# Performance work log

Hardware: AMD Instinct MI355X
Metric: run time of the kernel (lower is better)

## Reference

```python
import jax, jax.numpy as jnp
import numpy as np

TEMPERATURE = 0.08
NEG = -9e15  # matches torch masked_fill value
EPS = 1e-8   # F.cosine_similarity eps


def setup_inputs() -> dict:
    key = jax.random.key(0)
    inputs = jax.random.normal(key, (8192, 512), dtype=jnp.float32)
    return {"inputs": inputs}


def reference(inputs):
    N = inputs.shape[0]
    # cosine similarity via normalize + GEMM (avoids NxNxD broadcast)
    norms = jnp.maximum(jnp.linalg.norm(inputs, axis=-1, keepdims=True), EPS)
    z = inputs / norms
    sim = z @ z.T  # [N, N]
    # mask self-similarity BEFORE temperature scaling (as in the torch code)
    diag = jnp.eye(N, dtype=bool)
    sim = jnp.where(diag, NEG, sim)
    sim = sim / TEMPERATURE
    # positive of row i is column (i - N//2) % N (eye rolled by N//2 along dim 0)
    idx = jnp.arange(N)
    pos_idx = (idx - N // 2) % N
    pos = jnp.take_along_axis(sim, pos_idx[:, None], axis=1)[:, 0]  # [N]
    nll = jnp.mean(-pos + jax.scipy.special.logsumexp(sim, axis=-1))
    # rank of the positive: counting-based equivalent of
    # cat([pos, sim_masked]).argsort(desc).argmin() with stable ties
    masked = sim.at[idx, pos_idx].set(NEG)
    positive_ranking = jnp.sum(masked > pos[:, None], axis=-1)  # [N] int
    return positive_ranking, nll
```

## Files before the change

kernel.cpp:

```cpp
#include <hip/hip_runtime.h>
#include <cstdint>
#include <cstddef>

#define NROW 8192
#define DIM  512
#define HALF 4096
#define INV_T 12.5f
#define LDSW 64

typedef __bf16 bf16x8  __attribute__((ext_vector_type(8)));
typedef float  floatx4 __attribute__((ext_vector_type(4)));

__device__ __forceinline__ float bf2f_lo(unsigned u) { return __uint_as_float(u << 16); }
__device__ __forceinline__ float bf2f_hi(unsigned u) { return __uint_as_float(u & 0xffff0000u); }
__device__ __forceinline__ unsigned short f2bf(float f) {
    unsigned u = __float_as_uint(f);
    u += 0x7fffu + ((u >> 16) & 1u);
    return (unsigned short)(u >> 16);
}

__device__ __forceinline__ void atom_addf(float* p, float v) {
    __hip_atomic_fetch_add(p, v, __ATOMIC_RELAXED, __HIP_MEMORY_SCOPE_AGENT);
}

__global__ void knormpos(const float* __restrict__ x, unsigned short* __restrict__ z,
                         float* __restrict__ pos, float* __restrict__ sumexp,
                         float* __restrict__ cnt, float* __restrict__ nll_acc,
                         int* __restrict__ done) {
    int id = blockIdx.x * 256 + threadIdx.x;
    if (id < NROW) { sumexp[id] = 0.f; cnt[id] = 0.f; }
    if (id == 0) { nll_acc[0] = 0.f; done[0] = 0; }

    __shared__ __align__(16) unsigned short zs[4][512];

    const int w = threadIdx.x >> 6, lane = threadIdx.x & 63;
    const int row = blockIdx.x * 2 + (w & 1) + (w >> 1) * HALF;

    const float* xr = x + (size_t)row * DIM + lane * 8;
    float4 v0 = ((const float4*)xr)[0];
    float4 v1 = ((const float4*)xr)[1];
    float ss = v0.x*v0.x + v0.y*v0.y + v0.z*v0.z + v0.w*v0.w
             + v1.x*v1.x + v1.y*v1.y + v1.z*v1.z + v1.w*v1.w;
    #pragma unroll
    for (int m = 1; m < 64; m <<= 1) ss += __shfl_xor(ss, m);
    float inv = 1.0f / fmaxf(sqrtf(ss), 1e-8f);
    uint4 o;
    o.x = (unsigned)f2bf(v0.x * inv) | ((unsigned)f2bf(v0.y * inv) << 16);
    o.y = (unsigned)f2bf(v0.z * inv) | ((unsigned)f2bf(v0.w * inv) << 16);
    o.z = (unsigned)f2bf(v1.x * inv) | ((unsigned)f2bf(v1.y * inv) << 16);
    o.w = (unsigned)f2bf(v1.z * inv) | ((unsigned)f2bf(v1.w * inv) << 16);
    *(uint4*)(&zs[w][lane * 8]) = o;
    int sl = (lane & 56) | ((lane & 7) ^ (row & 7));
    *(uint4*)(z + (size_t)row * DIM + sl * 8) = o;
    __syncthreads();

    if (w < 2) {
        uint4 a = *(const uint4*)(&zs[w][lane * 8]);
        uint4 b = *(const uint4*)(&zs[w + 2][lane * 8]);
        float s = bf2f_lo(a.x)*bf2f_lo(b.x) + bf2f_hi(a.x)*bf2f_hi(b.x)
                + bf2f_lo(a.y)*bf2f_lo(b.y) + bf2f_hi(a.y)*bf2f_hi(b.y)
                + bf2f_lo(a.z)*bf2f_lo(b.z) + bf2f_hi(a.z)*bf2f_hi(b.z)
                + bf2f_lo(a.w)*bf2f_lo(b.w) + bf2f_hi(a.w)*bf2f_hi(b.w);
        #pragma unroll
        for (int m = 1; m < 64; m <<= 1) s += __shfl_xor(s, m);
        if (lane == 0) {
            const int r = blockIdx.x * 2 + w;
            pos[r] = s;
            pos[r + HALF] = s;
        }
    }
}

__global__ __launch_bounds__(256) void kgemm(const unsigned short* __restrict__ z,
                                             const float* __restrict__ pos,
                                             float* __restrict__ sumexp,
                                             float* __restrict__ cnt) {
    __shared__ __align__(16) unsigned short As[128 * LDSW];
    __shared__ __align__(16) unsigned short Bs[128 * LDSW];

    const int b = blockIdx.x;
    int I = 0;
    while (b >= 516 * (I + 1) - 32 * (I + 1) * (I + 1)) ++I;
    const int lb = b - (516 * I - 32 * I * I);
    int bi, bj;
    if (lb < 36) {
        int ti = 0;
        while (lb >= 8 * (ti + 1) - (ti + 1) * ti / 2) ++ti;
        const int tj = ti + (lb - (8 * ti - ti * (ti - 1) / 2));
        bi = I * 8 + ti;
        bj = I * 8 + tj;
    } else {
        const int o = lb - 36;
        const int J = I + 1 + (o >> 6);
        bi = I * 8 + ((o & 63) >> 3);
        bj = J * 8 + (o & 7);
    }
    const int r0 = bi * 128;
    const int c0 = bj * 128;
    const bool offdiag = (bi != bj);

    const int t = threadIdx.x;
    const int w = t >> 6, lane = t & 63;
    const int wm = w >> 1, wn = w & 1;

    floatx4 acc[4][4];
    #pragma unroll
    for (int i = 0; i < 4; ++i)
        #pragma unroll
        for (int j = 0; j < 4; ++j)
            acc[i][j] = floatx4{0.f, 0.f, 0.f, 0.f};

    const int lrow8 = lane >> 3;
    const int lcol  = (lane & 7) * 8;

    for (int kk = 0; kk < 8; ++kk) {
        const int k0 = kk * 64;
        #pragma unroll
        for (int it = 0; it < 4; ++it) {
            const int c = it * 4 + w;
            const unsigned short* gA = z + (size_t)(r0 + c * 8 + lrow8) * DIM + k0 + lcol;
            const unsigned short* gB = z + (size_t)(c0 + c * 8 + lrow8) * DIM + k0 + lcol;
            __builtin_amdgcn_global_load_lds(
                (const __attribute__((address_space(1))) unsigned int*)gA,
                (__attribute__((address_space(3))) unsigned int*)(As + c * 512),
                16, 0, 0);
            __builtin_amdgcn_global_load_lds(
                (const __attribute__((address_space(1))) unsigned int*)gB,
                (__attribute__((address_space(3))) unsigned int*)(Bs + c * 512),
                16, 0, 0);
        }
        __syncthreads();
        const int q = lane >> 4, cid16 = lane & 15;
        #pragma unroll
        for (int ks = 0; ks < 2; ++ks) {
            bf16x8 af[4], bfv[4];
            #pragma unroll
            for (int f = 0; f < 4; ++f) {
                const int ar = wm * 64 + f * 16 + cid16;
                const int br = wn * 64 + f * 16 + cid16;
                const int pa = (4 * ks + q) ^ (ar & 7);
                const int pb = (4 * ks + q) ^ (br & 7);
                af[f]  = *(const bf16x8*)(As + ar * LDSW + pa * 8);
                bfv[f] = *(const bf16x8*)(Bs + br * LDSW + pb * 8);
            }
            #pragma unroll
            for (int fm = 0; fm < 4; ++fm)
                #pragma unroll
                for (int fn = 0; fn < 4; ++fn)
                    acc[fm][fn] = __builtin_amdgcn_mfma_f32_16x16x32_bf16(
                        af[fm], bfv[fn], acc[fm][fn], 0, 0, 0);
        }
        __syncthreads();
    }

    const int rgrp = lane >> 4;
    const int cid  = lane & 15;

    #pragma unroll
    for (int fm = 0; fm < 4; ++fm) {
        #pragma unroll
        for (int r = 0; r < 4; ++r) {
            const int li = wm * 64 + fm * 16 + rgrp * 4 + r;
            const int i  = r0 + li;
            const float pv = pos[i];
            const int pj = (i + HALF) & (NROW - 1);
            float esum = 0.f, csum = 0.f;
            #pragma unroll
            for (int fn = 0; fn < 4; ++fn) {
                const int j = c0 + wn * 64 + fn * 16 + cid;
                const float s = acc[fm][fn][r];
                const bool diag = (j == i);
                esum += diag ? 0.f : __expf(s * INV_T - INV_T);
                csum += (!diag && (j != pj) && (s > pv)) ? 1.f : 0.f;
            }
            #pragma unroll
            for (int m = 1; m < 16; m <<= 1) {
                esum += __shfl_xor(esum, m);
                csum += __shfl_xor(csum, m);
            }
            if (cid == 0) {
                atom_addf(&sumexp[i], esum);
                atom_addf(&cnt[i], csum);
            }
        }
    }

    if (offdiag) {
        #pragma unroll
        for (int fn = 0; fn < 4; ++fn) {
            const int lj = wn * 64 + fn * 16 + cid;
            const int j  = c0 + lj;
            const float pvc = pos[j];
            const int pjc = (j + HALF) & (NROW - 1);
            float ec = 0.f, cc = 0.f;
            #pragma unroll
            for (int fm = 0; fm < 4; ++fm) {
                #pragma unroll
                for (int r = 0; r < 4; ++r) {
                    const int i = r0 + wm * 64 + fm * 16 + rgrp * 4 + r;
                    const float s = acc[fm][fn][r];
                    ec += __expf(s * INV_T - INV_T);
                    cc += ((i != pjc) && (s > pvc)) ? 1.f : 0.f;
                }
            }
            ec += __shfl_xor(ec, 16); ec += __shfl_xor(ec, 32);
            cc += __shfl_xor(cc, 16); cc += __shfl_xor(cc, 32);
            if (rgrp == 0) {
                atom_addf(&sumexp[j], ec);
                atom_addf(&cnt[j], cc);
            }
        }
    }
}

__global__ void NCELoss_3126736191777_kernel(const float* __restrict__ cnt,
                                             const float* __restrict__ sumexp,
                                             const float* __restrict__ pos,
                                             float* __restrict__ out,
                                             float* __restrict__ nll_acc,
                                             int* __restrict__ done) {
    __shared__ float red[4];
    const int t = threadIdx.x;
    const int r = blockIdx.x * 256 + t;
    float c = cnt[r], se = sumexp[r], p = pos[r];
    float v;
    if (p != p || fabsf(p) > 1.05f) v = 60000.0f;
    else if (se == 0.0f)            v = 40000.0f;
    else if (c < 0.0f)              v = 25000.0f;
    else                            v = c;
    out[r] = v;
    float local = -p * INV_T + INV_T + __logf(se);
    #pragma unroll
    for (int m = 1; m < 64; m <<= 1) local += __shfl_xor(local, m);
    if ((t & 63) == 0) red[t >> 6] = local;
    __syncthreads();
    if (t == 0) {
        atom_addf(nll_acc, red[0] + red[1] + red[2] + red[3]);
        __threadfence();
        int ticket = __hip_atomic_fetch_add(done, 1, __ATOMIC_ACQ_REL,
                                            __HIP_MEMORY_SCOPE_AGENT);
        if (ticket == (int)gridDim.x - 1) {
            __threadfence();
            out[NROW] = nll_acc[0] / (float)NROW;
        }
    }
}

extern "C" void kernel_launch(void* const* d_in, const int* in_sizes, int n_in,
                              void* d_out, int out_size, void* d_ws, size_t ws_size,
                              hipStream_t stream) {
    (void)in_sizes; (void)n_in; (void)out_size; (void)ws_size;
    const float* x = (const float*)d_in[0];

    char* base = (char*)d_ws;
    float* pos     = (float*)(base);
    float* sumexp  = (float*)(base + (size_t)NROW * 4);
    float* cnt     = (float*)(base + (size_t)NROW * 8);
    float* nll_acc = (float*)(base + (size_t)NROW * 12);
    int*   done    = (int*)(base + (size_t)NROW * 12 + 64);
    unsigned short* z = (unsigned short*)(base + (size_t)NROW * 12 + 4096);
    float* out = (float*)d_out;

    knormpos<<<NROW / 4, 256, 0, stream>>>(x, z, pos, sumexp, cnt, nll_acc, done);
    kgemm<<<2080, 256, 0, stream>>>(z, pos, sumexp, cnt);
    NCELoss_3126736191777_kernel<<<NROW / 256, 256, 0, stream>>>(cnt, sumexp, pos, out, nll_acc, done);
}
```

Baseline: 191.6 us.

## Load GEMM fragments directly from global memory and reduce row sums via LDS

The GEMM kernel drops its LDS staging and per-k-step barriers. Each lane now reads its bf16 MFMA fragments straight from global memory, and the swizzled z store is replaced by a plain row-major layout. The epilogue caches pos values in LDS and computes row and column exp/count partials in a single pass. Row partials are reduced through an LDS table so each row gets one atomic instead of one per 16-lane group. This removes barrier and LDS-copy overhead and cuts row atomics, but relies on L1/L2 for reuse, with 16-byte strided global loads that lose the shared-tile data reuse.

New measurement: 203.2 us. 6.0% more time.

```diff
diff --git a/kernel.cpp b/kernel.cpp
--- a/kernel.cpp
+++ b/kernel.cpp
@@ -6,7 +6,6 @@
 #define DIM  512
 #define HALF 4096
 #define INV_T 12.5f
-#define LDSW 64
 
 typedef __bf16 bf16x8  __attribute__((ext_vector_type(8)));
 typedef float  floatx4 __attribute__((ext_vector_type(4)));
@@ -50,8 +49,7 @@
     o.z = (unsigned)f2bf(v1.x * inv) | ((unsigned)f2bf(v1.y * inv) << 16);
     o.w = (unsigned)f2bf(v1.z * inv) | ((unsigned)f2bf(v1.w * inv) << 16);
     *(uint4*)(&zs[w][lane * 8]) = o;
-    int sl = (lane & 56) | ((lane & 7) ^ (row & 7));
-    *(uint4*)(z + (size_t)row * DIM + sl * 8) = o;
+    *(uint4*)(z + (size_t)row * DIM + lane * 8) = o;
     __syncthreads();
 
     if (w < 2) {
@@ -75,8 +73,10 @@
                                              const float* __restrict__ pos,
                                              float* __restrict__ sumexp,
                                              float* __restrict__ cnt) {
-    __shared__ __align__(16) unsigned short As[128 * LDSW];
-    __shared__ __align__(16) unsigned short Bs[128 * LDSW];
+    __shared__ float pos_r[128];
+    __shared__ float pos_c[128];
+    __shared__ float red_e[128][33];
+    __shared__ float red_c[128][33];
 
     const int b = blockIdx.x;
     int I = 0;
@@ -102,6 +102,18 @@
     const int t = threadIdx.x;
     const int w = t >> 6, lane = t & 63;
     const int wm = w >> 1, wn = w & 1;
+    const int cid = lane & 15, q = lane >> 4;
+
+    if (t < 128) pos_r[t] = pos[r0 + t];
+    else         pos_c[t - 128] = pos[c0 + (t - 128)];
+
+    const unsigned short* baseA[4];
+    const unsigned short* baseB[4];
+    #pragma unroll
+    for (int f = 0; f < 4; ++f) {
+        baseA[f] = z + (size_t)(r0 + wm * 64 + f * 16 + cid) * DIM + q * 8;
+        baseB[f] = z + (size_t)(c0 + wn * 64 + f * 16 + cid) * DIM + q * 8;
+    }
 
     floatx4 acc[4][4];
     #pragma unroll
@@ -110,38 +122,16 @@
         for (int j = 0; j < 4; ++j)
             acc[i][j] = floatx4{0.f, 0.f, 0.f, 0.f};
 
-    const int lrow8 = lane >> 3;
-    const int lcol  = (lane & 7) * 8;
-
+    #pragma unroll
     for (int kk = 0; kk < 8; ++kk) {
-        const int k0 = kk * 64;
-        #pragma unroll
-        for (int it = 0; it < 4; ++it) {
-            const int c = it * 4 + w;
-            const unsigned short* gA = z + (size_t)(r0 + c * 8 + lrow8) * DIM + k0 + lcol;
-            const unsigned short* gB = z + (size_t)(c0 + c * 8 + lrow8) * DIM + k0 + lcol;
-            __builtin_amdgcn_global_load_lds(
-                (const __attribute__((address_space(1))) unsigned int*)gA,
-                (__attribute__((address_space(3))) unsigned int*)(As + c * 512),
-                16, 0, 0);
-            __builtin_amdgcn_global_load_lds(
-                (const __attribute__((address_space(1))) unsigned int*)gB,
-                (__attribute__((address_space(3))) unsigned int*)(Bs + c * 512),
-                16, 0, 0);
-        }
-        __syncthreads();
-        const int q = lane >> 4, cid16 = lane & 15;
         #pragma unroll
         for (int ks = 0; ks < 2; ++ks) {
+            const int off = kk * 64 + ks * 32;
             bf16x8 af[4], bfv[4];
             #pragma unroll
             for (int f = 0; f < 4; ++f) {
-                const int ar = wm * 64 + f * 16 + cid16;
-                const int br = wn * 64 + f * 16 + cid16;
-                const int pa = (4 * ks + q) ^ (ar & 7);
-                const int pb = (4 * ks + q) ^ (br & 7);
-                af[f]  = *(const bf16x8*)(As + ar * LDSW + pa * 8);
-                bfv[f] = *(const bf16x8*)(Bs + br * LDSW + pb * 8);
+                af[f]  = *(const bf16x8*)(baseA[f] + off);
+                bfv[f] = *(const bf16x8*)(baseB[f] + off);
             }
             #pragma unroll
             for (int fm = 0; fm < 4; ++fm)
@@ -150,66 +140,63 @@
                     acc[fm][fn] = __builtin_amdgcn_mfma_f32_16x16x32_bf16(
                         af[fm], bfv[fn], acc[fm][fn], 0, 0, 0);
         }
-        __syncthreads();
-    }
-
-    const int rgrp = lane >> 4;
-    const int cid  = lane & 15;
-
+    }
+
+    __syncthreads();
+
+    float col_e[4] = {0.f, 0.f, 0.f, 0.f};
+    float col_c[4] = {0.f, 0.f, 0.f, 0.f};
     #pragma unroll
     for (int fm = 0; fm < 4; ++fm) {
         #pragma unroll
         for (int r = 0; r < 4; ++r) {
-            const int li = wm * 64 + fm * 16 + rgrp * 4 + r;
+            const int li = wm * 64 + fm * 16 + q * 4 + r;
             const int i  = r0 + li;
-            const float pv = pos[i];
+            const float pv = pos_r[li];
             const int pj = (i + HALF) & (NROW - 1);
-            float esum = 0.f, csum = 0.f;
+            float es = 0.f, cs = 0.f;
             #pragma unroll
             for (int fn = 0; fn < 4; ++fn) {
-                const int j = c0 + wn * 64 + fn * 16 + cid;
+                const int lj = wn * 64 + fn * 16 + cid;
+                const int j  = c0 + lj;
                 const float s = acc[fm][fn][r];
-                const bool diag = (j == i);
-                esum += diag ? 0.f : __expf(s * INV_T - INV_T);
-                csum += (!diag && (j != pj) && (s > pv)) ? 1.f : 0.f;
+                const float e = __expf((s - 1.0f) * INV_T);
+                const bool dg = (j == i);
+                es += dg ? 0.f : e;
+                cs += (!dg && (j != pj) && (s > pv)) ? 1.f : 0.f;
+                col_e[fn] += e;
+                const int pjc = (j + HALF) & (NROW - 1);
+                col_c[fn] += ((i != pjc) && (s > pos_c[lj])) ? 1.f : 0.f;
             }
-            #pragma unroll
-            for (int m = 1; m < 16; m <<= 1) {
-                esum += __shfl_xor(esum, m);
-                csum += __shfl_xor(csum, m);
-            }
-            if (cid == 0) {
-                atom_addf(&sumexp[i], esum);
-                atom_addf(&cnt[i], csum);
-            }
+            red_e[li][wn * 16 + cid] = es;
+            red_c[li][wn * 16 + cid] = cs;
         }
     }
 
     if (offdiag) {
         #pragma unroll
         for (int fn = 0; fn < 4; ++fn) {
-            const int lj = wn * 64 + fn * 16 + cid;
-            const int j  = c0 + lj;
-            const float pvc = pos[j];
-            const int pjc = (j + HALF) & (NROW - 1);
-            float ec = 0.f, cc = 0.f;
-            #pragma unroll
-            for (int fm = 0; fm < 4; ++fm) {
-                #pragma unroll
-                for (int r = 0; r < 4; ++r) {
-                    const int i = r0 + wm * 64 + fm * 16 + rgrp * 4 + r;
-                    const float s = acc[fm][fn][r];
-                    ec += __expf(s * INV_T - INV_T);
-                    cc += ((i != pjc) && (s > pvc)) ? 1.f : 0.f;
-                }
-            }
+            float ec = col_e[fn], cc = col_c[fn];
             ec += __shfl_xor(ec, 16); ec += __shfl_xor(ec, 32);
             cc += __shfl_xor(cc, 16); cc += __shfl_xor(cc, 32);
-            if (rgrp == 0) {
+            if (q == 0) {
+                const int j = c0 + wn * 64 + fn * 16 + cid;
                 atom_addf(&sumexp[j], ec);
                 atom_addf(&cnt[j], cc);
             }
         }
+    }
+
+    __syncthreads();
+
+    {
+        const int row = t >> 1;
+        float* src = (t & 1) ? &red_c[row][0] : &red_e[row][0];
+        float s = 0.f;
+        #pragma unroll
+        for (int c2 = 0; c2 < 32; ++c2) s += src[c2];
+        if (t & 1) atom_addf(&cnt[r0 + row], s);
+        else       atom_addf(&sumexp[r0 + row], s);
     }
 }
 
```

## Use 8 waves per GEMM tile and fuse row/column epilogue reductions

Applied to the files above, without the earlier changes.

Doubles the GEMM block to 512 threads so each wave owns a 32x64 sub-tile, which halves the accumulator registers per thread and is meant to raise occupancy and latency hiding. The row and column exp/count reductions now share one pass over the accumulators, so each exp is computed once instead of twice on off-diagonal tiles. Positive scores for the tile's rows and columns are staged in LDS. The trade-off is more waves per block loading the same tiles and extra atomics, since twice as many waves each issue per-row atomic adds.

New measurement: 166.0 us. -13.4%, faster.

```diff
diff --git a/kernel.cpp b/kernel.cpp
--- a/kernel.cpp
+++ b/kernel.cpp
@@ -71,12 +71,14 @@
     }
 }
 
-__global__ __launch_bounds__(256) void kgemm(const unsigned short* __restrict__ z,
-                                             const float* __restrict__ pos,
-                                             float* __restrict__ sumexp,
-                                             float* __restrict__ cnt) {
+__global__ __launch_bounds__(512, 3) void kgemm(const unsigned short* __restrict__ z,
+                                                const float* __restrict__ pos,
+                                                float* __restrict__ sumexp,
+                                                float* __restrict__ cnt) {
     __shared__ __align__(16) unsigned short As[128 * LDSW];
     __shared__ __align__(16) unsigned short Bs[128 * LDSW];
+    __shared__ float pos_r[128];
+    __shared__ float pos_c[128];
 
     const int b = blockIdx.x;
     int I = 0;
@@ -102,10 +104,14 @@
     const int t = threadIdx.x;
     const int w = t >> 6, lane = t & 63;
     const int wm = w >> 1, wn = w & 1;
-
-    floatx4 acc[4][4];
-    #pragma unroll
-    for (int i = 0; i < 4; ++i)
+    const int cid = lane & 15, q = lane >> 4;
+
+    if (t < 128) pos_r[t] = pos[r0 + t];
+    else if (t < 256) pos_c[t - 128] = pos[c0 + (t - 128)];
+
+    floatx4 acc[2][4];
+    #pragma unroll
+    for (int i = 0; i < 2; ++i)
         #pragma unroll
         for (int j = 0; j < 4; ++j)
             acc[i][j] = floatx4{0.f, 0.f, 0.f, 0.f};
@@ -116,8 +122,8 @@
     for (int kk = 0; kk < 8; ++kk) {
         const int k0 = kk * 64;
         #pragma unroll
-        for (int it = 0; it < 4; ++it) {
-            const int c = it * 4 + w;
+        for (int it = 0; it < 2; ++it) {
+            const int c = it * 8 + w;
             const unsigned short* gA = z + (size_t)(r0 + c * 8 + lrow8) * DIM + k0 + lcol;
             const unsigned short* gB = z + (size_t)(c0 + c * 8 + lrow8) * DIM + k0 + lcol;
             __builtin_amdgcn_global_load_lds(
@@ -130,21 +136,23 @@
                 16, 0, 0);
         }
         __syncthreads();
-        const int q = lane >> 4, cid16 = lane & 15;
         #pragma unroll
         for (int ks = 0; ks < 2; ++ks) {
-            bf16x8 af[4], bfv[4];
+            bf16x8 af[2], bfv[4];
+            #pragma unroll
+            for (int f = 0; f < 2; ++f) {
+                const int ar = wm * 32 + f * 16 + cid;
+                const int pa = (4 * ks + q) ^ (ar & 7);
+                af[f] = *(const bf16x8*)(As + ar * LDSW + pa * 8);
+            }
             #pragma unroll
             for (int f = 0; f < 4; ++f) {
-                const int ar = wm * 64 + f * 16 + cid16;
-                const int br = wn * 64 + f * 16 + cid16;
-                const int pa = (4 * ks + q) ^ (ar & 7);
+                const int br = wn * 64 + f * 16 + cid;
                 const int pb = (4 * ks + q) ^ (br & 7);
-                af[f]  = *(const bf16x8*)(As + ar * LDSW + pa * 8);
                 bfv[f] = *(const bf16x8*)(Bs + br * LDSW + pb * 8);
             }
             #pragma unroll
-            for (int fm = 0; fm < 4; ++fm)
+            for (int fm = 0; fm < 2; ++fm)
                 #pragma unroll
                 for (int fn = 0; fn < 4; ++fn)
                     acc[fm][fn] = __builtin_amdgcn_mfma_f32_16x16x32_bf16(
@@ -153,34 +161,38 @@
         __syncthreads();
     }
 
-    const int rgrp = lane >> 4;
-    const int cid  = lane & 15;
-
-    #pragma unroll
-    for (int fm = 0; fm < 4; ++fm) {
+    float col_e[4] = {0.f, 0.f, 0.f, 0.f};
+    float col_c[4] = {0.f, 0.f, 0.f, 0.f};
+    #pragma unroll
+    for (int fm = 0; fm < 2; ++fm) {
         #pragma unroll
         for (int r = 0; r < 4; ++r) {
-            const int li = wm * 64 + fm * 16 + rgrp * 4 + r;
+            const int li = wm * 32 + fm * 16 + q * 4 + r;
             const int i  = r0 + li;
-            const float pv = pos[i];
+            const float pv = pos_r[li];
             const int pj = (i + HALF) & (NROW - 1);
-            float esum = 0.f, csum = 0.f;
+            float es = 0.f, cs = 0.f;
             #pragma unroll
             for (int fn = 0; fn < 4; ++fn) {
-                const int j = c0 + wn * 64 + fn * 16 + cid;
+                const int lj = wn * 64 + fn * 16 + cid;
+                const int j  = c0 + lj;
                 const float s = acc[fm][fn][r];
-                const bool diag = (j == i);
-                esum += diag ? 0.f : __expf(s * INV_T - INV_T);
-                csum += (!diag && (j != pj) && (s > pv)) ? 1.f : 0.f;
+                const float e = __expf((s - 1.0f) * INV_T);
+                const bool dg = (j == i);
+                es += dg ? 0.f : e;
+                cs += (!dg && (j != pj) && (s > pv)) ? 1.f : 0.f;
+                col_e[fn] += e;
+                const int pjc = (j + HALF) & (NROW - 1);
+                col_c[fn] += ((i != pjc) && (s > pos_c[lj])) ? 1.f : 0.f;
             }
             #pragma unroll
             for (int m = 1; m < 16; m <<= 1) {
-                esum += __shfl_xor(esum, m);
-                csum += __shfl_xor(csum, m);
+                es += __shfl_xor(es, m);
+                cs += __shfl_xor(cs, m);
             }
             if (cid == 0) {
-                atom_addf(&sumexp[i], esum);
-                atom_addf(&cnt[i], csum);
+                atom_addf(&sumexp[i], es);
+                atom_addf(&cnt[i], cs);
             }
         }
     }
@@ -188,24 +200,11 @@
     if (offdiag) {
         #pragma unroll
         for (int fn = 0; fn < 4; ++fn) {
-            const int lj = wn * 64 + fn * 16 + cid;
-            const int j  = c0 + lj;
-            const float pvc = pos[j];
-            const int pjc = (j + HALF) & (NROW - 1);
-            float ec = 0.f, cc = 0.f;
-            #pragma unroll
-            for (int fm = 0; fm < 4; ++fm) {
-                #pragma unroll
-                for (int r = 0; r < 4; ++r) {
-                    const int i = r0 + wm * 64 + fm * 16 + rgrp * 4 + r;
-                    const float s = acc[fm][fn][r];
-                    ec += __expf(s * INV_T - INV_T);
-                    cc += ((i != pjc) && (s > pvc)) ? 1.f : 0.f;
-                }
-            }
+            float ec = col_e[fn], cc = col_c[fn];
             ec += __shfl_xor(ec, 16); ec += __shfl_xor(ec, 32);
             cc += __shfl_xor(cc, 16); cc += __shfl_xor(cc, 32);
-            if (rgrp == 0) {
+            if (q == 0) {
+                const int j = c0 + wn * 64 + fn * 16 + cid;
                 atom_addf(&sumexp[j], ec);
                 atom_addf(&cnt[j], cc);
             }
@@ -262,6 +261,6 @@
     float* out = (float*)d_out;
 
     knormpos<<<NROW / 4, 256, 0, stream>>>(x, z, pos, sumexp, cnt, nll_acc, done);
-    kgemm<<<2080, 256, 0, stream>>>(z, pos, sumexp, cnt);
+    kgemm<<<2080, 512, 0, stream>>>(z, pos, sumexp, cnt);
     NCELoss_3126736191777_kernel<<<NROW / 256, 256, 0, stream>>>(cnt, sumexp, pos, out, nll_acc, done);
 }
```
